# Kernel optimization log

Hardware: AMD Instinct MI355X
Metric: run time of the kernel (lower is better)

The kernel has to match this reference:

```python
import jax, jax.numpy as jnp
import numpy as np


def setup_inputs() -> dict:
    key = jax.random.key(0)
    k1, k2 = jax.random.split(key)
    b, feat = 8192, 256
    x = jax.random.normal(k1, (b, feat), dtype=jnp.float32)
    y = jax.random.randint(k2, (b,), 0, 100, dtype=jnp.int64)
    T = jnp.zeros((1,), dtype=jnp.float32)
    return {"x": x, "y": y, "T": T}


def reference(x, y, T):
    # SNNLoss.forward with inv=False, d=None, and no -1 labels in y
    b = x.shape[0]
    x = x / jnp.std(x, ddof=1)  # torch .std() is unbiased (ddof=1)

    # Pairwise Euclidean distance via Gram matrix (avoids [b,b,feat] blowup)
    sq = jnp.sum(x * x, axis=1)  # [b]
    d2 = jnp.maximum(sq[:, None] + sq[None, :] - 2.0 * (x @ x.T), 0.0)  # [b,b]
    eye = jnp.eye(b, dtype=bool)
    # diagonal is exactly 0 and masked out later; keep sqrt grad-safe there
    dist = jnp.where(eye, 0.0, jnp.sqrt(jnp.where(eye, 1.0, d2)))

    e_dist = -dist * jnp.power(jnp.float32(10.0), T[0])  # [b,b]
    neg_inf = jnp.float32(-jnp.inf)

    # denominator: all pairs except self
    den_dist = jnp.where(eye, neg_inf, e_dist)
    den = jax.scipy.special.logsumexp(den_dist, axis=1)  # [b]

    # numerator: same-label pairs except self
    m_num = (y[:, None] == y[None, :]) & ~eye  # [b,b]
    has = jnp.any(m_num, axis=1)  # rows with at least one positive
    num_dist = jnp.where(m_num, e_dist, neg_inf)
    # rows with no positives would give logsumexp = -inf; torch code zeroes
    # both num and den there. Substitute finite values, then zero the term.
    num = jax.scipy.special.logsumexp(jnp.where(has[:, None], num_dist, 0.0), axis=1)
    terms = jnp.where(has, num - den, 0.0)
    return -jnp.mean(terms)
```

## Files before the change

kernel.cpp:

```cpp
#include <hip/hip_runtime.h>

#define B_ROWS 8192
#define FEAT   256
#define NCH    8
#define CH_COLS 1024
#define NJT    16

typedef float f32x4 __attribute__((ext_vector_type(4)));
typedef _Float16 f16x8 __attribute__((ext_vector_type(8)));

typedef const __attribute__((address_space(1))) unsigned int* gas_ptr;
typedef __attribute__((address_space(3))) unsigned int* las_ptr;

__device__ __forceinline__ void gload_lds16(const void* g, void* l) {
  __builtin_amdgcn_global_load_lds((gas_ptr)g, (las_ptr)l, 16, 0, 0);
}

__global__ __launch_bounds__(256) void prep_kernel(
    const float* __restrict__ x, unsigned short* __restrict__ xh,
    float* __restrict__ sq, float* __restrict__ part_s,
    float* __restrict__ part_q)
{
  int tid = threadIdx.x;
  int l = tid & 63, wid = tid >> 6;
  int row = blockIdx.x * 4 + wid;
  const float4* xv = (const float4*)(x + (size_t)row * FEAT);
  float4 v = xv[l];
  ushort4 u;
  u.x = __builtin_bit_cast(unsigned short, (_Float16)v.x);
  u.y = __builtin_bit_cast(unsigned short, (_Float16)v.y);
  u.z = __builtin_bit_cast(unsigned short, (_Float16)v.z);
  u.w = __builtin_bit_cast(unsigned short, (_Float16)v.w);
  ((ushort4*)(xh + (size_t)row * FEAT))[l] = u;
  float ssq  = v.x*v.x + v.y*v.y + v.z*v.z + v.w*v.w;
  float ssum = v.x + v.y + v.z + v.w;
  #pragma unroll
  for (int m = 32; m; m >>= 1) {
    ssq  += __shfl_xor(ssq, m);
    ssum += __shfl_xor(ssum, m);
  }
  if (l == 0) sq[row] = ssq;
  __shared__ float red[8];
  if (l == 0) { red[wid*2] = ssum; red[wid*2+1] = ssq; }
  __syncthreads();
  if (tid == 0) {
    part_s[blockIdx.x] = red[0]+red[2]+red[4]+red[6];
    part_q[blockIdx.x] = red[1]+red[3]+red[5]+red[7];
  }
}

template<bool DIAG>
__device__ __forceinline__ void epilogue(
    const f32x4 (&acc)[2][4], const float* __restrict__ sq,
    const int* __restrict__ y, int j0, int l15,
    int i0q, const float (&sqi)[8], const int (&yiv)[8],
    float (&sden)[8], float (&snum)[8], float nscale2)
{
  int jb = j0 + l15;
  float sqj[4]; int yj[4];
  #pragma unroll
  for (int cb = 0; cb < 4; ++cb) {
    int j = jb + cb*16;
    sqj[cb] = sq[j];
    yj[cb]  = y[j];
  }
  #pragma unroll
  for (int rb = 0; rb < 2; ++rb) {
    #pragma unroll
    for (int r = 0; r < 4; ++r) {
      float si = sqi[rb*4+r];
      int   ig = i0q + rb*16 + r;
      int   yi = yiv[rb*4+r];
      float dacc = 0.f, nacc = 0.f;
      #pragma unroll
      for (int cb = 0; cb < 4; ++cb) {
        float S  = acc[rb][cb][r];
        float d2 = fmaf(S, -2.0f, si + sqj[cb]);
        d2 = fmaxf(d2, 0.0f);
        float e  = __builtin_amdgcn_exp2f(__builtin_amdgcn_sqrtf(d2) * nscale2);
        bool offd = !DIAG || (ig != jb + cb*16);
        dacc += offd ? e : 0.0f;
        nacc += (yi == yj[cb] && offd) ? e : 0.0f;
      }
      sden[rb*4+r] += dacc;
      snum[rb*4+r] += nacc;
    }
  }
}

__global__ __launch_bounds__(256, 2) void snn_main(
    const unsigned short* __restrict__ xh, const float* __restrict__ sq,
    const int* __restrict__ y, const float* __restrict__ T,
    const float* __restrict__ part_s, const float* __restrict__ part_q,
    float* __restrict__ pden, float* __restrict__ pnum)
{
  __shared__ __align__(16) char lB[32768];
  int tid = threadIdx.x;
  int l = tid & 63, wid = tid >> 6;
  int quad = l >> 4, l15 = l & 15;
  int l5 = l >> 5, s31 = l & 31;
  int ch = blockIdx.x, it = blockIdx.y;
  int i0 = it * 128, chbase = ch * CH_COLS;
  const char* xbc = (const char*)xh;

  f16x8 areg[2][8];
  #pragma unroll
  for (int rb = 0; rb < 2; ++rb)
    #pragma unroll
    for (int kk = 0; kk < 8; ++kk)
      areg[rb][kk] = *(const f16x8*)(xbc +
          (size_t)(i0 + wid*32 + rb*16 + l15)*512 + kk*64 + quad*16);

  float s_acc = 0.f, q_acc = 0.f;
  #pragma unroll
  for (int t = 0; t < 32; ++t) {
    s_acc += part_s[l + 64*t];
    q_acc += part_q[l + 64*t];
  }
  #pragma unroll
  for (int m = 1; m <= 32; m <<= 1) {
    s_acc += __shfl_xor(s_acc, m);
    q_acc += __shfl_xor(q_acc, m);
  }
  const double n = (double)B_ROWS * FEAT;
  double var = ((double)q_acc - (double)s_acc*(double)s_acc/n) / (n - 1.0);
  float stdv = (float)sqrt(var);
  float p10  = __builtin_amdgcn_exp2f(T[0] * 3.3219280948873623f);
  float nscale2 = -(p10 * 1.4426950408889634f / stdv);

  float sqi[8]; int yiv[8];
  int i0q = i0 + wid*32 + quad*4;
  #pragma unroll
  for (int rb = 0; rb < 2; ++rb)
    #pragma unroll
    for (int r = 0; r < 4; ++r) {
      int idx = i0q + rb*16 + r;
      sqi[rb*4+r] = sq[idx];
      yiv[rb*4+r] = y[idx];
    }

  float sden[8], snum[8];
  #pragma unroll
  for (int v = 0; v < 8; ++v) { sden[v] = 0.f; snum[v] = 0.f; }
  f32x4 acc[2][4];
  const f32x4 zero4 = {0.f, 0.f, 0.f, 0.f};

  for (int jt = 0; jt < NJT; ++jt) {
    int j0 = chbase + jt * 64;

    __syncthreads();
    {
      const char* gB = xbc + (size_t)j0 * 512;
      #pragma unroll
      for (int s = 0; s < 8; ++s) {
        int c  = wid*8 + s;
        int rw = 2*c + l5;
        int gg = s31 ^ (rw & 7);
        gload_lds16(gB + rw*512 + gg*16, lB + c*1024);
      }
    }

    if (jt > 0) {
      int pj0 = j0 - 64;
      if (pj0 == i0 || pj0 == i0 + 64)
        epilogue<true >(acc, sq, y, pj0, l15, i0q, sqi, yiv, sden, snum, nscale2);
      else
        epilogue<false>(acc, sq, y, pj0, l15, i0q, sqi, yiv, sden, snum, nscale2);
    }
    #pragma unroll
    for (int rb = 0; rb < 2; ++rb)
      #pragma unroll
      for (int cb = 0; cb < 4; ++cb)
        acc[rb][cb] = zero4;

    __syncthreads();

    #pragma unroll
    for (int kk = 0; kk < 8; ++kk) {
      f16x8 bv[4];
      #pragma unroll
      for (int cb = 0; cb < 4; ++cb) {
        int nr = cb*16 + l15;
        bv[cb] = *(const f16x8*)(lB + nr*512 + ((((kk<<2)|quad) ^ (l15 & 7)) << 4));
      }
      #pragma unroll
      for (int rb = 0; rb < 2; ++rb)
        #pragma unroll
        for (int cb = 0; cb < 4; ++cb)
          acc[rb][cb] = __builtin_amdgcn_mfma_f32_16x16x32_f16(areg[rb][kk], bv[cb], acc[rb][cb], 0, 0, 0);
    }
  }
  {
    int pj0 = chbase + (NJT-1) * 64;
    if (pj0 == i0 || pj0 == i0 + 64)
      epilogue<true >(acc, sq, y, pj0, l15, i0q, sqi, yiv, sden, snum, nscale2);
    else
      epilogue<false>(acc, sq, y, pj0, l15, i0q, sqi, yiv, sden, snum, nscale2);
  }

  #pragma unroll
  for (int v = 0; v < 8; ++v) {
    #pragma unroll
    for (int m = 1; m <= 8; m <<= 1) {
      sden[v] += __shfl_xor(sden[v], m);
      snum[v] += __shfl_xor(snum[v], m);
    }
  }
  if (l15 == 0) {
    int base = (it*NCH + ch) * 128;
    #pragma unroll
    for (int rb = 0; rb < 2; ++rb)
      #pragma unroll
      for (int r = 0; r < 4; ++r) {
        int rin = wid*32 + rb*16 + quad*4 + r;
        pden[base + rin] = sden[rb*4+r];
        pnum[base + rin] = snum[rb*4+r];
      }
  }
}

__global__ __launch_bounds__(1024) void final_kernel(
    const float* __restrict__ pden, const float* __restrict__ pnum,
    float* __restrict__ out)
{
  int tid = threadIdx.x;
  float tot = 0.f;
  #pragma unroll
  for (int rr = 0; rr < 8; ++rr) {
    int row = tid + 1024*rr;
    int itt = row >> 7, rin = row & 127;
    float den = 0.f, num = 0.f;
    #pragma unroll
    for (int p = 0; p < NCH; ++p) {
      den += pden[(itt*NCH + p)*128 + rin];
      num += pnum[(itt*NCH + p)*128 + rin];
    }
    if (num > 0.f)
      tot += 0.6931471805599453f *
             (__builtin_amdgcn_logf(num) - __builtin_amdgcn_logf(den));
  }
  #pragma unroll
  for (int m = 32; m; m >>= 1) tot += __shfl_xor(tot, m);
  __shared__ float red[16];
  if ((tid & 63) == 0) red[tid >> 6] = tot;
  __syncthreads();
  if (tid == 0) {
    float s = 0.f;
    #pragma unroll
    for (int w = 0; w < 16; ++w) s += red[w];
    out[0] = -s / 8192.0f;
  }
}

extern "C" void kernel_launch(void* const* d_in, const int* in_sizes, int n_in,
                              void* d_out, int out_size, void* d_ws, size_t ws_size,
                              hipStream_t stream)
{
  (void)in_sizes; (void)n_in; (void)out_size; (void)ws_size;
  const float* x  = (const float*)d_in[0];
  const int* y    = (const int*)d_in[1];
  const float* T  = (const float*)d_in[2];
  char* ws = (char*)d_ws;
  float* part_s = (float*)(ws + 1024);
  float* part_q = (float*)(ws + 1024 + 8192);
  float* sq     = (float*)(ws + 32768);
  unsigned short* xh = (unsigned short*)(ws + 65536);
  float* pden   = (float*)(ws + 65536 + 4194304);
  float* pnum   = pden + 64*NCH*128;

  hipLaunchKernelGGL(prep_kernel, dim3(B_ROWS/4), dim3(256), 0, stream,
                     x, xh, sq, part_s, part_q);
  hipLaunchKernelGGL(snn_main, dim3(NCH, B_ROWS/128), dim3(256), 0, stream,
                     xh, sq, y, T, part_s, part_q, pden, pnum);
  hipLaunchKernelGGL(final_kernel, dim3(1), dim3(1024), 0, stream,
                     pden, pnum, (float*)d_out);
}
```

Before: 120.6 us.

## Double-buffer LDS B tiles to prefetch the next column tile

The single 32KB LDS B buffer becomes two 32KB buffers. The global-to-LDS load for the next 64-column tile is issued right after the loop's one barrier, so it overlaps with the epilogue and the MFMA work on the current tile. The second __syncthreads per iteration is removed, and the swizzled LDS read offsets are precomputed once outside the loop. LDS per block doubles to 64KB, which could limit occupancy at two blocks per CU.

Result: slower. 123.3 us (+2.2%).

```diff
diff --git a/kernel.cpp b/kernel.cpp
--- a/kernel.cpp
+++ b/kernel.cpp
@@ -94,7 +94,7 @@
     const float* __restrict__ part_s, const float* __restrict__ part_q,
     float* __restrict__ pden, float* __restrict__ pnum)
 {
-  __shared__ __align__(16) char lB[32768];
+  __shared__ __align__(16) char lB[65536];
   int tid = threadIdx.x;
   int l = tid & 63, wid = tid >> 6;
   int quad = l >> 4, l15 = l & 15;
@@ -139,29 +139,50 @@
       yiv[rb*4+r] = y[idx];
     }
 
+  int bbase[4][2];
+  #pragma unroll
+  for (int cb = 0; cb < 4; ++cb)
+    #pragma unroll
+    for (int kl = 0; kl < 2; ++kl)
+      bbase[cb][kl] = (cb*16 + l15)*512 +
+                      ((((kl<<2)|quad) ^ (l15 & 7)) << 4);
+
   float sden[8], snum[8];
   #pragma unroll
   for (int v = 0; v < 8; ++v) { sden[v] = 0.f; snum[v] = 0.f; }
   f32x4 acc[2][4];
   const f32x4 zero4 = {0.f, 0.f, 0.f, 0.f};
 
+  {
+    const char* gB = xbc + (size_t)chbase * 512;
+    #pragma unroll
+    for (int s = 0; s < 8; ++s) {
+      int c  = wid*8 + s;
+      int rw = 2*c + l5;
+      int gg = s31 ^ (rw & 7);
+      gload_lds16(gB + rw*512 + gg*16, lB + c*1024);
+    }
+  }
+
   for (int jt = 0; jt < NJT; ++jt) {
-    int j0 = chbase + jt * 64;
+    const char* lb = lB + ((jt & 1) << 15);
 
     __syncthreads();
-    {
-      const char* gB = xbc + (size_t)j0 * 512;
+
+    if (jt + 1 < NJT) {
+      char* ldst = lB + (((jt + 1) & 1) << 15);
+      const char* gB = xbc + (size_t)(chbase + (jt + 1) * 64) * 512;
       #pragma unroll
       for (int s = 0; s < 8; ++s) {
         int c  = wid*8 + s;
         int rw = 2*c + l5;
         int gg = s31 ^ (rw & 7);
-        gload_lds16(gB + rw*512 + gg*16, lB + c*1024);
+        gload_lds16(gB + rw*512 + gg*16, ldst + c*1024);
       }
     }
 
     if (jt > 0) {
-      int pj0 = j0 - 64;
+      int pj0 = chbase + (jt - 1) * 64;
       if (pj0 == i0 || pj0 == i0 + 64)
         epilogue<true >(acc, sq, y, pj0, l15, i0q, sqi, yiv, sden, snum, nscale2);
       else
@@ -173,16 +194,12 @@
       for (int cb = 0; cb < 4; ++cb)
         acc[rb][cb] = zero4;
 
-    __syncthreads();
-
     #pragma unroll
     for (int kk = 0; kk < 8; ++kk) {
       f16x8 bv[4];
       #pragma unroll
-      for (int cb = 0; cb < 4; ++cb) {
-        int nr = cb*16 + l15;
-        bv[cb] = *(const f16x8*)(lB + nr*512 + ((((kk<<2)|quad) ^ (l15 & 7)) << 4));
-      }
+      for (int cb = 0; cb < 4; ++cb)
+        bv[cb] = *(const f16x8*)(lb + bbase[cb][kk & 1] + ((kk >> 1) << 7));
       #pragma unroll
       for (int rb = 0; rb < 2; ++rb)
         #pragma unroll
@@ -191,7 +208,7 @@
     }
   }
   {
-    int pj0 = chbase + (NJT-1) * 64;
+    int pj0 = chbase + (NJT - 1) * 64;
     if (pj0 == i0 || pj0 == i0 + 64)
       epilogue<true >(acc, sq, y, pj0, l15, i0q, sqi, yiv, sden, snum, nscale2);
     else
```
